# Kernel tuning notes

Hardware: AMD Instinct MI355X
Metric: run time of the kernel (lower is better)

The kernel has to match this reference:

```python
import jax, jax.numpy as jnp
import numpy as np

B, L, D, H, DH, DL, NB = 8, 1024, 512, 8, 64, 64, 128
EPS = 1e-6


def layer_norm(x, g, b):
    m = jnp.mean(x, axis=-1, keepdims=True)
    v = jnp.mean((x - m) ** 2, axis=-1, keepdims=True)
    return (x - m) * jax.lax.rsqrt(v + EPS) * g + b


def rel_bias(timestamps, pos_w, ts_w):
    # position part: skew trick, pos_w has length 2L-1
    t = jnp.concatenate([pos_w, jnp.zeros((L,), pos_w.dtype)])  # (3L-1,)
    t = jnp.tile(t, L)[:-L].reshape(L, 3 * L - 2)
    rel_pos = t[:, L - 1:2 * L - 1]  # (L, L)
    # timestamp part: bucketized pairwise diffs of extended timestamps
    ext = jnp.concatenate([timestamps, timestamps[:, L - 1:L]], axis=1)  # (B, L+1)
    d = ext[:, 1:, None] - ext[:, None, :-1]  # (B, L, L)
    mag = jnp.maximum(jnp.abs(d).astype(jnp.float32), 1.0)
    bucket = jnp.clip((jnp.log(mag) / 0.301).astype(jnp.int32), 0, NB)
    rel_ts = ts_w[bucket]  # (B, L, L)
    return rel_pos[None] + rel_ts


def setup_inputs() -> dict:
    key = jax.random.key(0)
    ks = jax.random.split(key, 8)
    x = jax.random.normal(ks[0], (B, L, D), dtype=jnp.float32)
    timestamps = jnp.sort(jax.random.randint(ks[1], (B, L), 0, 1000000, dtype=jnp.int64), axis=1)
    attn_mask = jnp.triu(jnp.ones((L, L), jnp.float32), k=1)[None, None]  # 1 = masked (future)
    total_out = 2 * DL * H + 2 * DH * H
    uvqk_w = jax.random.normal(ks[2], (D, total_out), dtype=jnp.float32) * 0.02
    out_w = jax.random.normal(ks[3], (DL * H, D), dtype=jnp.float32) * 0.02
    out_b = jnp.zeros((D,), jnp.float32)
    ln1_g = jnp.ones((D,), jnp.float32); ln1_b = jnp.zeros((D,), jnp.float32)
    ln2_g = jnp.ones((DL * H,), jnp.float32); ln2_b = jnp.zeros((DL * H,), jnp.float32)
    ts_weights = jax.random.normal(ks[4], (NB + 1,), dtype=jnp.float32) * 0.02
    pos_weights = jax.random.normal(ks[5], (2 * L - 1,), dtype=jnp.float32) * 0.02
    return {"x": x, "timestamps": timestamps, "attn_mask": attn_mask,
            "uvqk_w": uvqk_w, "out_w": out_w, "out_b": out_b,
            "ln1_g": ln1_g, "ln1_b": ln1_b, "ln2_g": ln2_g, "ln2_b": ln2_b,
            "ts_weights": ts_weights, "pos_weights": pos_weights}


def reference(x, timestamps, attn_mask, uvqk_w, out_w, out_b,
              ln1_g, ln1_b, ln2_g, ln2_b, ts_weights, pos_weights):
    z = layer_norm(x, ln1_g, ln1_b)
    z = jax.nn.silu(z @ uvqk_w)  # linear_activation == 'silu'
    u, v, q, k = jnp.split(z, [DL * H, 2 * DL * H, 2 * DL * H + DH * H], axis=-1)
    q = q.reshape(B, L, H, DH)
    k = k.reshape(B, L, H, DH)
    v = v.reshape(B, L, H, DL)
    scores = jnp.einsum('bmhd,bnhd->bhmn', q, k)
    scores = scores + rel_bias(timestamps, pos_weights, ts_weights)[:, None]
    scores = jax.nn.silu(scores) / L * (1.0 - attn_mask)
    z = jnp.einsum('bhmn,bnhd->bmhd', scores, v).reshape(B, L, H * DL)
    z = layer_norm(z, ln2_g, ln2_b) * u  # gated LN
    return z @ out_w + out_b + x
```

## Files before the change

### kernel.cpp

```cpp
#include <hip/hip_runtime.h>
#include <math.h>

constexpr int Bc = 8;
constexpr int Lc = 1024;
constexpr int Dc = 512;
constexpr int Hc = 8;
constexpr int DHc = 64;
constexpr int DLc = 64;
constexpr int NBc = 128;
constexpr int TOTAL_OUT = 2 * DLc * Hc + 2 * DHc * Hc;
constexpr int ROWS = Bc * Lc;

using f32x4 = __attribute__((ext_vector_type(4))) float;
using s16x8 = __attribute__((ext_vector_type(8))) short;

__device__ __forceinline__ float bf2f(ushort u) {
    union { unsigned int i; float f; } v; v.i = ((unsigned int)u) << 16; return v.f;
}
__device__ __forceinline__ ushort f2bf(float f) {
    union { float f; unsigned int i; } v; v.f = f;
    unsigned int r = v.i + 0x7fffu + ((v.i >> 16) & 1u);
    return (ushort)(r >> 16);
}
__device__ __forceinline__ float silu(float x) {
    float e = __expf(-x);
    return x * __builtin_amdgcn_rcpf(1.0f + e);
}

__global__ __launch_bounds__(256) void transpose_cast(const float* __restrict__ in,
                                                      ushort* __restrict__ out,
                                                      int R, int C) {
    __shared__ float tile[32][33];
    int bc = blockIdx.x * 32, br = blockIdx.y * 32;
    int tx = threadIdx.x & 31, ty = threadIdx.x >> 5;
    for (int i = ty; i < 32; i += 8) {
        int r = br + i, c = bc + tx;
        tile[i][tx] = (r < R && c < C) ? in[(size_t)r * C + c] : 0.f;
    }
    __syncthreads();
    for (int i = ty; i < 32; i += 8) {
        int c = bc + i, r = br + tx;
        if (c < C && r < R) out[(size_t)c * R + r] = f2bf(tile[tx][i]);
    }
}

__global__ __launch_bounds__(256) void ln1_kernel(const float* __restrict__ x,
                                                  const float* __restrict__ g,
                                                  const float* __restrict__ bta,
                                                  ushort* __restrict__ outp) {
    int wid = threadIdx.x >> 6, lane = threadIdx.x & 63;
    int row = blockIdx.x * 4 + wid;
    const float4* xr = (const float4*)(x + (size_t)row * Dc);
    float4 a = xr[lane * 2], c = xr[lane * 2 + 1];
    float xv[8] = {a.x, a.y, a.z, a.w, c.x, c.y, c.z, c.w};
    float s = 0.f, q = 0.f;
#pragma unroll
    for (int i = 0; i < 8; i++) { s += xv[i]; q += xv[i] * xv[i]; }
#pragma unroll
    for (int off = 32; off; off >>= 1) { s += __shfl_xor(s, off); q += __shfl_xor(q, off); }
    float mean = s * (1.f / 512.f);
    float var  = q * (1.f / 512.f) - mean * mean;
    float rstd = rsqrtf(var + 1e-6f);
    const float4* gv = (const float4*)g; const float4* bv = (const float4*)bta;
    float4 g0 = gv[lane * 2], g1 = gv[lane * 2 + 1];
    float4 b0 = bv[lane * 2], b1 = bv[lane * 2 + 1];
    float G[8] = {g0.x, g0.y, g0.z, g0.w, g1.x, g1.y, g1.z, g1.w};
    float Bv[8] = {b0.x, b0.y, b0.z, b0.w, b1.x, b1.y, b1.z, b1.w};
    union { ushort u16[8]; uint4 v; } pk;
#pragma unroll
    for (int i = 0; i < 8; i++) pk.u16[i] = f2bf((xv[i] - mean) * rstd * G[i] + Bv[i]);
    ((uint4*)(outp + (size_t)row * Dc))[lane] = pk.v;
}

__global__ __launch_bounds__(256) void gemm1_kernel(const ushort* __restrict__ A,
                                                    const ushort* __restrict__ Bt,
                                                    ushort* __restrict__ Ub,
                                                    ushort* __restrict__ VTg,
                                                    ushort* __restrict__ Qb,
                                                    ushort* __restrict__ Kb) {
    __shared__ __align__(16) ushort As[128][72];
    __shared__ __align__(16) ushort Bs[128][72];
    int tid = threadIdx.x;
    int m0 = blockIdx.x * 128, n0 = blockIdx.y * 128;
    int w = tid >> 6, lane = tid & 63;
    int wm = (w >> 1) * 64, wn = (w & 1) * 64;
    f32x4 acc[4][4] = {};
    for (int k0 = 0; k0 < Dc; k0 += 64) {
        __syncthreads();
#pragma unroll
        for (int c = tid; c < 1024; c += 256) {
            int r = c >> 3, c8 = c & 7;
            *(uint4*)&As[r][c8 * 8] = *(const uint4*)&A[(size_t)(m0 + r) * Dc + k0 + c8 * 8];
            *(uint4*)&Bs[r][c8 * 8] = *(const uint4*)&Bt[(size_t)(n0 + r) * Dc + k0 + c8 * 8];
        }
        __syncthreads();
#pragma unroll
        for (int ks = 0; ks < 2; ++ks) {
            int kb = ks * 32 + (lane >> 4) * 8;
            s16x8 af[4], bfr[4];
#pragma unroll
            for (int i = 0; i < 4; i++) af[i] = *(const s16x8*)&As[wm + i * 16 + (lane & 15)][kb];
#pragma unroll
            for (int j = 0; j < 4; j++) bfr[j] = *(const s16x8*)&Bs[wn + j * 16 + (lane & 15)][kb];
#pragma unroll
            for (int i = 0; i < 4; i++)
#pragma unroll
                for (int j = 0; j < 4; j++)
                    acc[i][j] = __builtin_amdgcn_mfma_f32_16x16x32_bf16(af[i], bfr[j], acc[i][j], 0, 0, 0);
        }
    }
    int lr = (lane >> 4) * 4, lc = lane & 15;
#pragma unroll
    for (int i = 0; i < 4; i++)
#pragma unroll
        for (int j = 0; j < 4; j++) {
            int col = n0 + wn + j * 16 + lc;
            int sect = col >> 9, cc = col & 511;
            int row0 = m0 + wm + i * 16 + lr;
            if (sect == 1) {
                int hh = cc >> 6, dd = cc & 63;
                int bb = row0 >> 10, nn = row0 & 1023;
                ushort4 pk;
                pk.x = f2bf(silu(acc[i][j][0]));
                pk.y = f2bf(silu(acc[i][j][1]));
                pk.z = f2bf(silu(acc[i][j][2]));
                pk.w = f2bf(silu(acc[i][j][3]));
                *(ushort4*)&VTg[((size_t)((bb * 8 + hh) * 64 + dd)) * 1024 + nn] = pk;
            } else {
                ushort* dst = (sect == 0) ? Ub : (sect == 2) ? Qb : Kb;
#pragma unroll
                for (int r = 0; r < 4; r++)
                    dst[(size_t)(row0 + r) * 512 + cc] = f2bf(silu(acc[i][j][r]));
            }
        }
}

__global__ __launch_bounds__(256, 3) void attn_kernel(const ushort* __restrict__ Qb,
                                                      const ushort* __restrict__ Kb,
                                                      const ushort* __restrict__ VTg,
                                                      const int* __restrict__ ts,
                                                      const float* __restrict__ pos_w,
                                                      const float* __restrict__ ts_w,
                                                      ushort* __restrict__ Ob) {
    int bx = blockIdx.x;
    int mt = (bx & 1) ? (bx >> 1) : (15 - (bx >> 1));
    int h = blockIdx.y, b = blockIdx.z;
    __shared__ __align__(16) ushort Ks[2][64][64];
    __shared__ __align__(16) ushort Ps[4][16][72];
    __shared__ float posw[2 * Lc - 1];
    __shared__ float tsw[NBc + 1];
    __shared__ int tss[Lc];
    int tid = threadIdx.x, w = tid >> 6, lane = tid & 63;
    const size_t qkbase = ((size_t)b * Lc) * 512 + h * 64;
    const size_t vtbase = ((size_t)((b * 8 + h) * 64)) * 1024;
    const int m0 = mt * 64;
    for (int i = tid; i < 2 * Lc - 1; i += 256) posw[i] = pos_w[i];
    for (int i = tid; i < Lc; i += 256) tss[i] = ts[b * Lc + i];
    if (tid < NBc + 1) tsw[tid] = ts_w[tid];

    int lc = lane & 15, g4 = lane >> 4;
    int lr = g4 * 4;
    int sr = tid >> 2;
    int ss0 = (tid & 3) * 2;
    const ushort* kgrow = Kb + qkbase + (size_t)sr * 512;
    int dso0 = sr * 64 + (((ss0)     ^ (sr & 7)) * 8);
    int dso1 = sr * 64 + (((ss0 + 1) ^ (sr & 7)) * 8);

    {
        uint4 ka = *(const uint4*)(kgrow + ss0 * 8);
        uint4 kb_ = *(const uint4*)(kgrow + (ss0 + 1) * 8);
        *(uint4*)&(&Ks[0][0][0])[dso0] = ka;
        *(uint4*)&(&Ks[0][0][0])[dso1] = kb_;
    }
    __syncthreads();

    s16x8 qf[2];
#pragma unroll
    for (int ks = 0; ks < 2; ++ks)
        qf[ks] = *(const s16x8*)&Qb[qkbase + (size_t)(m0 + w * 16 + lc) * 512 + ks * 32 + g4 * 8];
    int mbase = m0 + w * 16 + lr;
    int me_r[4];
#pragma unroll
    for (int r = 0; r < 4; r++) {
        int mp = mbase + r + 1;
        me_r[r] = tss[mp < Lc ? mp : (Lc - 1)];
    }

    f32x4 acc_o[4] = {};
    int ntiles = mt + 1;
    int cur = 0;
    for (int nt = 0; nt < ntiles; ++nt) {
        int n0 = nt * 64;
        s16x8 vb[2][4];
#pragma unroll
        for (int ks = 0; ks < 2; ++ks)
#pragma unroll
            for (int j = 0; j < 4; j++)
                vb[ks][j] = *(const s16x8*)&VTg[vtbase + (size_t)(j * 16 + lc) * 1024 + n0 + ks * 32 + g4 * 8];
        bool hasnext = (nt + 1 < ntiles);
        uint4 ka = {}, kb_ = {};
        if (hasnext) {
            const ushort* kgn = kgrow + (size_t)(n0 + 64) * 512;
            ka  = *(const uint4*)(kgn + ss0 * 8);
            kb_ = *(const uint4*)(kgn + (ss0 + 1) * 8);
        }
        const ushort* ksb = &Ks[cur][0][0];
        f32x4 s[4] = {};
#pragma unroll
        for (int ks = 0; ks < 2; ++ks) {
            s16x8 kf[4];
#pragma unroll
            for (int j = 0; j < 4; j++)
                kf[j] = *(const s16x8*)&ksb[(j * 16 + lc) * 64 + (((ks * 4 + g4) ^ (lc & 7)) * 8)];
#pragma unroll
            for (int j = 0; j < 4; j++)
                s[j] = __builtin_amdgcn_mfma_f32_16x16x32_bf16(qf[ks], kf[j], s[j], 0, 0, 0);
        }
#pragma unroll
        for (int j = 0; j < 4; j++) {
            int ncol = n0 + j * 16 + lc;
            int tn = tss[ncol];
#pragma unroll
            for (int r = 0; r < 4; r++) {
                int m = mbase + r;
                float val = 0.f;
                if (ncol <= m) {
                    float mag = fmaxf(fabsf((float)(me_r[r] - tn)), 1.f);
                    int bkt = (int)(__log2f(mag) * 2.3028147f);
                    bkt = bkt < 0 ? 0 : (bkt > NBc ? NBc : bkt);
                    float sv = s[j][r] + posw[(Lc - 1) + ncol - m] + tsw[bkt];
                    val = silu(sv) * (1.f / (float)Lc);
                }
                Ps[w][lr + r][j * 16 + lc] = f2bf(val);
            }
        }
#pragma unroll
        for (int ks = 0; ks < 2; ++ks) {
            s16x8 pa = *(const s16x8*)&Ps[w][lc][ks * 32 + g4 * 8];
#pragma unroll
            for (int j = 0; j < 4; j++)
                acc_o[j] = __builtin_amdgcn_mfma_f32_16x16x32_bf16(pa, vb[ks][j], acc_o[j], 0, 0, 0);
        }
        if (hasnext) {
            ushort* kd = &Ks[cur ^ 1][0][0];
            *(uint4*)&kd[dso0] = ka;
            *(uint4*)&kd[dso1] = kb_;
        }
        __syncthreads();
        cur ^= 1;
    }
#pragma unroll
    for (int j = 0; j < 4; j++)
#pragma unroll
        for (int r = 0; r < 4; r++) {
            int m = mbase + r;
            Ob[qkbase + (size_t)m * 512 + j * 16 + lc] = f2bf(acc_o[j][r]);
        }
}

__global__ __launch_bounds__(256) void ln2_kernel(const ushort* __restrict__ z,
                                                  const ushort* __restrict__ u,
                                                  const float* __restrict__ g,
                                                  const float* __restrict__ bta,
                                                  ushort* __restrict__ outp) {
    int wid = threadIdx.x >> 6, lane = threadIdx.x & 63;
    int row = blockIdx.x * 4 + wid;
    uint4 zv = ((const uint4*)(z + (size_t)row * 512))[lane];
    ushort* zu = (ushort*)&zv;
    float xv[8], s = 0.f, q = 0.f;
#pragma unroll
    for (int i = 0; i < 8; i++) { xv[i] = bf2f(zu[i]); s += xv[i]; q += xv[i] * xv[i]; }
#pragma unroll
    for (int off = 32; off; off >>= 1) { s += __shfl_xor(s, off); q += __shfl_xor(q, off); }
    float mean = s * (1.f / 512.f);
    float var  = q * (1.f / 512.f) - mean * mean;
    float rstd = rsqrtf(var + 1e-6f);
    uint4 uv = ((const uint4*)(u + (size_t)row * 512))[lane];
    ushort* uu = (ushort*)&uv;
    const float4* gv = (const float4*)g; const float4* bv = (const float4*)bta;
    float4 g0 = gv[lane * 2], g1 = gv[lane * 2 + 1];
    float4 b0 = bv[lane * 2], b1 = bv[lane * 2 + 1];
    float G[8] = {g0.x, g0.y, g0.z, g0.w, g1.x, g1.y, g1.z, g1.w};
    float Bv[8] = {b0.x, b0.y, b0.z, b0.w, b1.x, b1.y, b1.z, b1.w};
    union { ushort u16[8]; uint4 v; } pk;
#pragma unroll
    for (int i = 0; i < 8; i++)
        pk.u16[i] = f2bf(((xv[i] - mean) * rstd * G[i] + Bv[i]) * bf2f(uu[i]));
    ((uint4*)(outp + (size_t)row * 512))[lane] = pk.v;
}

__global__ __launch_bounds__(256) void gemm2_kernel(const ushort* __restrict__ A,
                                                    const ushort* __restrict__ Bt,
                                                    const float* __restrict__ ob,
                                                    const float* __restrict__ x,
                                                    float* __restrict__ outp) {
    __shared__ __align__(16) ushort As[128][72];
    __shared__ __align__(16) ushort Bs[128][72];
    int tid = threadIdx.x;
    int m0 = blockIdx.x * 128, n0 = blockIdx.y * 128;
    int w = tid >> 6, lane = tid & 63;
    int wm = (w >> 1) * 64, wn = (w & 1) * 64;
    f32x4 acc[4][4] = {};
    for (int k0 = 0; k0 < Dc; k0 += 64) {
        __syncthreads();
#pragma unroll
        for (int c = tid; c < 1024; c += 256) {
            int r = c >> 3, c8 = c & 7;
            *(uint4*)&As[r][c8 * 8] = *(const uint4*)&A[(size_t)(m0 + r) * Dc + k0 + c8 * 8];
            *(uint4*)&Bs[r][c8 * 8] = *(const uint4*)&Bt[(size_t)(n0 + r) * Dc + k0 + c8 * 8];
        }
        __syncthreads();
#pragma unroll
        for (int ks = 0; ks < 2; ++ks) {
            int kb = ks * 32 + (lane >> 4) * 8;
            s16x8 af[4], bfr[4];
#pragma unroll
            for (int i = 0; i < 4; i++) af[i] = *(const s16x8*)&As[wm + i * 16 + (lane & 15)][kb];
#pragma unroll
            for (int j = 0; j < 4; j++) bfr[j] = *(const s16x8*)&Bs[wn + j * 16 + (lane & 15)][kb];
#pragma unroll
            for (int i = 0; i < 4; i++)
#pragma unroll
                for (int j = 0; j < 4; j++)
                    acc[i][j] = __builtin_amdgcn_mfma_f32_16x16x32_bf16(af[i], bfr[j], acc[i][j], 0, 0, 0);
        }
    }
    int lr = (lane >> 4) * 4, lc = lane & 15;
#pragma unroll
    for (int i = 0; i < 4; i++)
#pragma unroll
        for (int j = 0; j < 4; j++) {
            int col = n0 + wn + j * 16 + lc;
            float bias = ob[col];
#pragma unroll
            for (int r = 0; r < 4; r++) {
                int row = m0 + wm + i * 16 + lr + r;
                size_t off = (size_t)row * 512 + col;
                outp[off] = acc[i][j][r] + bias + x[off];
            }
        }
}

extern "C" void kernel_launch(void* const* d_in, const int* in_sizes, int n_in,
                              void* d_out, int out_size, void* d_ws, size_t ws_size,
                              hipStream_t stream) {
    const float* x      = (const float*)d_in[0];
    const int*   tsp    = (const int*)d_in[1];
    const float* uvqk_w = (const float*)d_in[3];
    const float* out_w  = (const float*)d_in[4];
    const float* out_b  = (const float*)d_in[5];
    const float* ln1_g  = (const float*)d_in[6];
    const float* ln1_b  = (const float*)d_in[7];
    const float* ln2_g  = (const float*)d_in[8];
    const float* ln2_b  = (const float*)d_in[9];
    const float* ts_w   = (const float*)d_in[10];
    const float* pos_w  = (const float*)d_in[11];
    float* outp = (float*)d_out;

    char* ws = (char*)d_ws;
    size_t off = 0;
    auto alloc = [&](size_t bytes) { char* p = ws + off; off += (bytes + 255) & ~(size_t)255; return p; };
    const size_t MAT = (size_t)ROWS * 512 * sizeof(ushort);
    ushort* W1T = (ushort*)alloc((size_t)TOTAL_OUT * Dc * 2);
    ushort* W2T = (ushort*)alloc((size_t)Dc * Dc * 2);
    ushort* X1  = (ushort*)alloc(MAT);
    ushort* Ub  = (ushort*)alloc(MAT);
    ushort* VTg = (ushort*)alloc(MAT);
    ushort* Qb  = (ushort*)alloc(MAT);
    ushort* Kb  = (ushort*)alloc(MAT);
    ushort* Ob  = (ushort*)alloc(MAT);
    ushort* A2  = X1;

    transpose_cast<<<dim3(TOTAL_OUT / 32, Dc / 32), 256, 0, stream>>>(uvqk_w, W1T, Dc, TOTAL_OUT);
    transpose_cast<<<dim3(Dc / 32, Dc / 32), 256, 0, stream>>>(out_w, W2T, Dc, Dc);
    ln1_kernel<<<ROWS / 4, 256, 0, stream>>>(x, ln1_g, ln1_b, X1);
    gemm1_kernel<<<dim3(ROWS / 128, TOTAL_OUT / 128), 256, 0, stream>>>(X1, W1T, Ub, VTg, Qb, Kb);
    attn_kernel<<<dim3(16, Hc, Bc), 256, 0, stream>>>(Qb, Kb, VTg, tsp, pos_w, ts_w, Ob);
    ln2_kernel<<<ROWS / 4, 256, 0, stream>>>(Ob, Ub, ln2_g, ln2_b, A2);
    gemm2_kernel<<<dim3(ROWS / 128, Dc / 128), 256, 0, stream>>>(A2, W2T, out_b, x, outp);
}
```

Baseline: 259.2 us.

## Precompute head-shared relative bias into bf16 buffer in a separate kernel

Adds a bias kernel that computes the position plus bucketized timestamp bias once per batch (shared across all 8 heads) and stores it as a bf16 B×L×L buffer. The attention kernel then loads the bias per tile instead of recomputing log2 bucketing and shared-memory table lookups per head, and applies the causal mask only on the diagonal tile. This removes repeated transcendental and LDS work and shared-memory staging, which lifts occupancy limits. In exchange it adds 16 MB of bias writes and per-head global reads with a strided, uncoalesced 2-byte access pattern, plus bf16 rounding of the bias.

```diff
diff --git a/kernel.cpp b/kernel.cpp
--- a/kernel.cpp
+++ b/kernel.cpp
@@ -70,6 +70,41 @@
 #pragma unroll
     for (int i = 0; i < 8; i++) pk.u16[i] = f2bf((xv[i] - mean) * rstd * G[i] + Bv[i]);
     ((uint4*)(outp + (size_t)row * Dc))[lane] = pk.v;
+}
+
+__global__ __launch_bounds__(256) void bias_kernel(const int* __restrict__ ts,
+                                                   const float* __restrict__ pos_w,
+                                                   const float* __restrict__ ts_w,
+                                                   ushort* __restrict__ biasb) {
+    __shared__ float posw[2 * Lc - 1];
+    __shared__ float tsw[NBc + 1];
+    int tid = threadIdx.x;
+    int b = blockIdx.y;
+    for (int i = tid; i < 2 * Lc - 1; i += 256) posw[i] = pos_w[i];
+    if (tid < NBc + 1) tsw[tid] = ts_w[tid];
+    __syncthreads();
+    int m = blockIdx.x * 8 + (tid >> 5);
+    int n0 = (tid & 31) * 32;
+    const int* tsb = ts + b * Lc;
+    int mp = m + 1 < Lc ? m + 1 : Lc - 1;
+    int tsm = tsb[mp];
+    int pbase = (Lc - 1) + n0 - m;
+    union { ushort u16[32]; uint4 v[4]; } o;
+#pragma unroll
+    for (int i = 0; i < 32; i += 4) {
+        int4 tn = *(const int4*)&tsb[n0 + i];
+        int dv[4] = {tsm - tn.x, tsm - tn.y, tsm - tn.z, tsm - tn.w};
+#pragma unroll
+        for (int e = 0; e < 4; e++) {
+            float mag = fmaxf(fabsf((float)dv[e]), 1.f);
+            int bkt = (int)(__log2f(mag) * 2.3028147f);
+            bkt = bkt < 0 ? 0 : (bkt > NBc ? NBc : bkt);
+            o.u16[i + e] = f2bf(posw[pbase + i + e] + tsw[bkt]);
+        }
+    }
+    uint4* dst = (uint4*)&biasb[((size_t)b * Lc + m) * Lc + n0];
+#pragma unroll
+    for (int i = 0; i < 4; i++) dst[i] = o.v[i];
 }
 
 __global__ __launch_bounds__(256) void gemm1_kernel(const ushort* __restrict__ A,
@@ -135,31 +170,22 @@
         }
 }
 
-__global__ __launch_bounds__(256, 3) void attn_kernel(const ushort* __restrict__ Qb,
-                                                      const ushort* __restrict__ Kb,
-                                                      const ushort* __restrict__ VTg,
-                                                      const int* __restrict__ ts,
-                                                      const float* __restrict__ pos_w,
-                                                      const float* __restrict__ ts_w,
-                                                      ushort* __restrict__ Ob) {
+__global__ __launch_bounds__(256) void attn_kernel(const ushort* __restrict__ Qb,
+                                                   const ushort* __restrict__ Kb,
+                                                   const ushort* __restrict__ VTg,
+                                                   const ushort* __restrict__ biasb,
+                                                   ushort* __restrict__ Ob) {
     int bx = blockIdx.x;
     int mt = (bx & 1) ? (bx >> 1) : (15 - (bx >> 1));
     int h = blockIdx.y, b = blockIdx.z;
     __shared__ __align__(16) ushort Ks[2][64][64];
     __shared__ __align__(16) ushort Ps[4][16][72];
-    __shared__ float posw[2 * Lc - 1];
-    __shared__ float tsw[NBc + 1];
-    __shared__ int tss[Lc];
     int tid = threadIdx.x, w = tid >> 6, lane = tid & 63;
     const size_t qkbase = ((size_t)b * Lc) * 512 + h * 64;
     const size_t vtbase = ((size_t)((b * 8 + h) * 64)) * 1024;
+    const ushort* biasB = biasb + (size_t)b * Lc * Lc;
     const int m0 = mt * 64;
-    for (int i = tid; i < 2 * Lc - 1; i += 256) posw[i] = pos_w[i];
-    for (int i = tid; i < Lc; i += 256) tss[i] = ts[b * Lc + i];
-    if (tid < NBc + 1) tsw[tid] = ts_w[tid];
-
-    int lc = lane & 15, g4 = lane >> 4;
-    int lr = g4 * 4;
+    int lc = lane & 15, g4 = lane >> 4, lr = g4 * 4;
     int sr = tid >> 2;
     int ss0 = (tid & 3) * 2;
     const ushort* kgrow = Kb + qkbase + (size_t)sr * 512;
@@ -179,12 +205,6 @@
     for (int ks = 0; ks < 2; ++ks)
         qf[ks] = *(const s16x8*)&Qb[qkbase + (size_t)(m0 + w * 16 + lc) * 512 + ks * 32 + g4 * 8];
     int mbase = m0 + w * 16 + lr;
-    int me_r[4];
-#pragma unroll
-    for (int r = 0; r < 4; r++) {
-        int mp = mbase + r + 1;
-        me_r[r] = tss[mp < Lc ? mp : (Lc - 1)];
-    }
 
     f32x4 acc_o[4] = {};
     int ntiles = mt + 1;
@@ -197,6 +217,12 @@
 #pragma unroll
             for (int j = 0; j < 4; j++)
                 vb[ks][j] = *(const s16x8*)&VTg[vtbase + (size_t)(j * 16 + lc) * 1024 + n0 + ks * 32 + g4 * 8];
+        ushort bsv[4][4];
+#pragma unroll
+        for (int j = 0; j < 4; j++)
+#pragma unroll
+            for (int r = 0; r < 4; r++)
+                bsv[j][r] = biasB[(size_t)(mbase + r) * Lc + n0 + j * 16 + lc];
         bool hasnext = (nt + 1 < ntiles);
         uint4 ka = {}, kb_ = {};
         if (hasnext) {
@@ -216,24 +242,16 @@
             for (int j = 0; j < 4; j++)
                 s[j] = __builtin_amdgcn_mfma_f32_16x16x32_bf16(qf[ks], kf[j], s[j], 0, 0, 0);
         }
-#pragma unroll
-        for (int j = 0; j < 4; j++) {
-            int ncol = n0 + j * 16 + lc;
-            int tn = tss[ncol];
+        bool diag = (nt == mt);
+#pragma unroll
+        for (int j = 0; j < 4; j++)
 #pragma unroll
             for (int r = 0; r < 4; r++) {
-                int m = mbase + r;
-                float val = 0.f;
-                if (ncol <= m) {
-                    float mag = fmaxf(fabsf((float)(me_r[r] - tn)), 1.f);
-                    int bkt = (int)(__log2f(mag) * 2.3028147f);
-                    bkt = bkt < 0 ? 0 : (bkt > NBc ? NBc : bkt);
-                    float sv = s[j][r] + posw[(Lc - 1) + ncol - m] + tsw[bkt];
-                    val = silu(sv) * (1.f / (float)Lc);
-                }
+                float sv = s[j][r] + bf2f(bsv[j][r]);
+                float val = silu(sv) * (1.f / (float)Lc);
+                if (diag && (j * 16 + lc) > (w * 16 + lr + r)) val = 0.f;
                 Ps[w][lr + r][j * 16 + lc] = f2bf(val);
             }
-        }
 #pragma unroll
         for (int ks = 0; ks < 2; ++ks) {
             s16x8 pa = *(const s16x8*)&Ps[w][lc][ks * 32 + g4 * 8];
@@ -369,13 +387,15 @@
     ushort* Qb  = (ushort*)alloc(MAT);
     ushort* Kb  = (ushort*)alloc(MAT);
     ushort* Ob  = (ushort*)alloc(MAT);
+    ushort* BIAS = (ushort*)alloc((size_t)Bc * Lc * Lc * 2);
     ushort* A2  = X1;
 
     transpose_cast<<<dim3(TOTAL_OUT / 32, Dc / 32), 256, 0, stream>>>(uvqk_w, W1T, Dc, TOTAL_OUT);
     transpose_cast<<<dim3(Dc / 32, Dc / 32), 256, 0, stream>>>(out_w, W2T, Dc, Dc);
+    bias_kernel<<<dim3(Lc / 8, Bc), 256, 0, stream>>>(tsp, pos_w, ts_w, BIAS);
     ln1_kernel<<<ROWS / 4, 256, 0, stream>>>(x, ln1_g, ln1_b, X1);
     gemm1_kernel<<<dim3(ROWS / 128, TOTAL_OUT / 128), 256, 0, stream>>>(X1, W1T, Ub, VTg, Qb, Kb);
-    attn_kernel<<<dim3(16, Hc, Bc), 256, 0, stream>>>(Qb, Kb, VTg, tsp, pos_w, ts_w, Ob);
+    attn_kernel<<<dim3(16, Hc, Bc), 256, 0, stream>>>(Qb, Kb, VTg, BIAS, Ob);
     ln2_kernel<<<ROWS / 4, 256, 0, stream>>>(Ob, Ub, ln2_g, ln2_b, A2);
     gemm2_kernel<<<dim3(ROWS / 128, Dc / 128), 256, 0, stream>>>(A2, W2T, out_b, x, outp);
 }
```

After: 274.7 us. 6.0% more time.
